# Optimization experiments

Measured on AMD Instinct MI355X. Metric: run time of the kernel, lower is better.

Reference implementation:

```python
import jax, jax.numpy as jnp
import numpy as np

BATCH = 4096
INDIM = 1024
OUTDIM = 1024
NNZ = 52224  # min(1024,1024) * int(1024 * 0.05)


def setup_inputs() -> dict:
    key = jax.random.key(0)
    k1, k2, k3, k4, k5 = jax.random.split(key, 5)
    stdv = np.sqrt(2.0 / INDIM).astype(np.float32)
    input_ = jax.random.normal(k1, (BATCH, INDIM), dtype=jnp.float32)
    weight = jax.random.normal(k2, (NNZ,), dtype=jnp.float32) * stdv
    bias = jax.random.normal(k3, (OUTDIM,), dtype=jnp.float32) * stdv
    ind_in = jax.random.randint(k4, (NNZ,), 0, INDIM, dtype=jnp.int32)
    ind_out = jax.random.randint(k5, (NNZ,), 0, OUTDIM, dtype=jnp.int32)
    return {"input_": input_, "weight": weight, "bias": bias,
            "ind_in": ind_in, "ind_out": ind_out}


def reference(input_, weight, bias, ind_in, ind_out):
    # x = input_[:, ind_in] * weight        [B, NNZ]
    gathered = input_[:, ind_in] * weight
    # scatter_add into output columns       [B, OUTDIM]
    out = jnp.zeros((input_.shape[0], OUTDIM), dtype=input_.dtype)
    out = out.at[:, ind_out].add(gathered)
    return out + bias
```

## Files before the change

### kernel.cpp

```cpp
#include <hip/hip_runtime.h>
#include <stdint.h>

#define INDIM   1024
#define OUTDIM  1024
#define BM 64
#define BN 64
#define BK 64
#define KTILES (INDIM / BK)

typedef __attribute__((ext_vector_type(8))) short  short8;
typedef __attribute__((ext_vector_type(4))) float  floatx4;

__global__ void k_scatter_w(const int* __restrict__ ind_in, const int* __restrict__ ind_out,
                            const float* __restrict__ w, float* __restrict__ W32T, int nnz) {
    int k = blockIdx.x * 256 + threadIdx.x;
    if (k < nnz)
        atomicAdd(&W32T[(size_t)ind_out[k] * INDIM + ind_in[k]], w[k]);
}

__device__ __forceinline__ uint32_t bf16pack(float x, float y) {
    uint32_t ux = __float_as_uint(x);
    ux = ((ux + 0x7FFFu + ((ux >> 16) & 1u)) >> 16) & 0xFFFFu;
    uint32_t uy = __float_as_uint(y);
    uy = (uy + 0x7FFFu + ((uy >> 16) & 1u)) & 0xFFFF0000u;
    return ux | uy;
}

__global__ void k_convert(const float4* __restrict__ A, uint2* __restrict__ A16, int nA4,
                          const float4* __restrict__ Wt, uint2* __restrict__ W16, int nW4) {
    int i = blockIdx.x * 256 + threadIdx.x;
    int stride = gridDim.x * 256;
    for (int j = i; j < nA4; j += stride) {
        float4 v = A[j];
        A16[j] = make_uint2(bf16pack(v.x, v.y), bf16pack(v.z, v.w));
    }
    for (int j = i; j < nW4; j += stride) {
        float4 v = Wt[j];
        W16[j] = make_uint2(bf16pack(v.x, v.y), bf16pack(v.z, v.w));
    }
}

__global__ __launch_bounds__(256, 4) void k_gemm(
    const ushort* __restrict__ A16,
    const ushort* __restrict__ W16T,
    const float* __restrict__ bias,
    float* __restrict__ C, int M)
{
    __shared__ ushort lA[BM * BK];
    __shared__ ushort lB[BN * BK];

    const int t      = threadIdx.x;
    const int w      = t >> 6;
    const int L      = t & 63;
    const int lane15 = L & 15;
    const int lane7  = L & 7;
    const int quad   = L >> 4;
    const int wm     = w >> 1, wn = w & 1;

    const int bid = blockIdx.x;
    const int bm0 = ((bid & 7) * 8 + (bid >> 7)) * BM;
    const int bn0 = ((bid >> 3) & 15) * BN;

    const int srow = t >> 3;
    const int j8   = (t & 7) ^ (srow & 7);

    const ushort* Abase = A16  + (size_t)bm0 * INDIM;
    const ushort* Bbase = W16T + (size_t)bn0 * INDIM;

    floatx4 acc[2][2] = {};

    for (int kt = 0; kt < KTILES; ++kt) {
        const int gcol = kt * BK + j8 * 8;
        uint4 va0 = *(const uint4*)(Abase + (size_t)srow        * INDIM + gcol);
        uint4 va1 = *(const uint4*)(Abase + (size_t)(srow + 32) * INDIM + gcol);
        uint4 vb0 = *(const uint4*)(Bbase + (size_t)srow        * INDIM + gcol);
        uint4 vb1 = *(const uint4*)(Bbase + (size_t)(srow + 32) * INDIM + gcol);
        __syncthreads();
        *(uint4*)(lA + (size_t)t * 8)         = va0;
        *(uint4*)(lA + (size_t)(t + 256) * 8) = va1;
        *(uint4*)(lB + (size_t)t * 8)         = vb0;
        *(uint4*)(lB + (size_t)(t + 256) * 8) = vb1;
        __syncthreads();

        #pragma unroll
        for (int ks = 0; ks < 2; ++ks) {
            const int koff = (((ks * 4 + quad) ^ lane7) * 8);
            short8 af[2], bf[2];
            #pragma unroll
            for (int tm = 0; tm < 2; ++tm)
                af[tm] = *(const short8*)(lA + (wm * 32 + tm * 16 + lane15) * 64 + koff);
            #pragma unroll
            for (int tn = 0; tn < 2; ++tn)
                bf[tn] = *(const short8*)(lB + (wn * 32 + tn * 16 + lane15) * 64 + koff);
            #pragma unroll
            for (int tm = 0; tm < 2; ++tm)
                #pragma unroll
                for (int tn = 0; tn < 2; ++tn)
                    acc[tm][tn] = __builtin_amdgcn_mfma_f32_16x16x32_bf16(
                        af[tm], bf[tn], acc[tm][tn], 0, 0, 0);
        }
    }

    #pragma unroll
    for (int tm = 0; tm < 2; ++tm) {
        #pragma unroll
        for (int tn = 0; tn < 2; ++tn) {
            const int col = bn0 + wn * 32 + tn * 16 + lane15;
            const float bv = bias[col];
            #pragma unroll
            for (int r = 0; r < 4; ++r) {
                const int row = bm0 + wm * 32 + tm * 16 + quad * 4 + r;
                C[(size_t)row * OUTDIM + col] = acc[tm][tn][r] + bv;
            }
        }
    }
}

extern "C" void kernel_launch(void* const* d_in, const int* in_sizes, int n_in,
                              void* d_out, int out_size, void* d_ws, size_t ws_size,
                              hipStream_t stream) {
    const float* input  = (const float*)d_in[0];
    const float* weight = (const float*)d_in[1];
    const float* bias   = (const float*)d_in[2];
    const int*   ind_in  = (const int*)d_in[3];
    const int*   ind_out = (const int*)d_in[4];
    float* out = (float*)d_out;

    const int nnz = in_sizes[1];
    const int M   = out_size / OUTDIM;

    char* ws = (char*)d_ws;
    float*  W32T = (float*)ws;
    ushort* W16T = (ushort*)(ws + (4u << 20));
    ushort* A16  = (ushort*)(ws + (6u << 20));

    (void)hipMemsetAsync(W32T, 0, (size_t)OUTDIM * INDIM * sizeof(float), stream);
    k_scatter_w<<<(nnz + 255) / 256, 256, 0, stream>>>(ind_in, ind_out, weight, W32T, nnz);
    k_convert<<<2048, 256, 0, stream>>>((const float4*)input, (uint2*)A16, M * INDIM / 4,
                                        (const float4*)W32T, (uint2*)W16T, OUTDIM * INDIM / 4);
    k_gemm<<<(M / BM) * (OUTDIM / BN), 256, 0, stream>>>(A16, W16T, bias, out, M);
}
```

Measured before the change: 99.61 us.

## Fuse weight scatter and bf16 conversion via grid barrier; use direct-to-LDS loads

Merges the scatter-add and the conversion kernels into one persistent-style kernel of 1024 blocks. The blocks synchronise through a global atomic counter barrier, which removes one launch. The GEMM now stages tiles with global_load_lds, so data goes straight to LDS without passing through registers, and the output uses nontemporal stores. The grid barrier requires all 1024 blocks to be co-resident, and it assumes nnz fits within the 256K threads.

```diff
diff --git a/kernel.cpp b/kernel.cpp
--- a/kernel.cpp
+++ b/kernel.cpp
@@ -7,16 +7,10 @@
 #define BN 64
 #define BK 64
 #define KTILES (INDIM / BK)
+#define PREP_BLOCKS 1024
 
 typedef __attribute__((ext_vector_type(8))) short  short8;
 typedef __attribute__((ext_vector_type(4))) float  floatx4;
-
-__global__ void k_scatter_w(const int* __restrict__ ind_in, const int* __restrict__ ind_out,
-                            const float* __restrict__ w, float* __restrict__ W32T, int nnz) {
-    int k = blockIdx.x * 256 + threadIdx.x;
-    if (k < nnz)
-        atomicAdd(&W32T[(size_t)ind_out[k] * INDIM + ind_in[k]], w[k]);
-}
 
 __device__ __forceinline__ uint32_t bf16pack(float x, float y) {
     uint32_t ux = __float_as_uint(x);
@@ -26,18 +20,42 @@
     return ux | uy;
 }
 
-__global__ void k_convert(const float4* __restrict__ A, uint2* __restrict__ A16, int nA4,
-                          const float4* __restrict__ Wt, uint2* __restrict__ W16, int nW4) {
-    int i = blockIdx.x * 256 + threadIdx.x;
-    int stride = gridDim.x * 256;
-    for (int j = i; j < nA4; j += stride) {
-        float4 v = A[j];
+__global__ __launch_bounds__(256) void k_prep(
+    const int* __restrict__ ind_in, const int* __restrict__ ind_out,
+    const float* __restrict__ wgt, int nnz,
+    const float4* __restrict__ A32, int nA4,
+    float* __restrict__ W32T, uint2* __restrict__ W16T, uint2* __restrict__ A16,
+    unsigned* __restrict__ barrier_ctr)
+{
+    const int gtid = blockIdx.x * 256 + threadIdx.x;
+
+    if (gtid < nnz)
+        atomicAdd(&W32T[(size_t)ind_out[gtid] * INDIM + ind_in[gtid]], wgt[gtid]);
+
+    __threadfence();
+    __syncthreads();
+    if (threadIdx.x == 0) {
+        __hip_atomic_fetch_add(barrier_ctr, 1u, __ATOMIC_RELEASE, __HIP_MEMORY_SCOPE_AGENT);
+        while (__hip_atomic_load(barrier_ctr, __ATOMIC_ACQUIRE, __HIP_MEMORY_SCOPE_AGENT)
+               < (unsigned)PREP_BLOCKS)
+            __builtin_amdgcn_s_sleep(4);
+    }
+    __syncthreads();
+
+    {
+        float4 v = ((const float4*)W32T)[gtid];
+        W16T[gtid] = make_uint2(bf16pack(v.x, v.y), bf16pack(v.z, v.w));
+    }
+    for (int j = gtid; j < nA4; j += PREP_BLOCKS * 256) {
+        float4 v = A32[j];
         A16[j] = make_uint2(bf16pack(v.x, v.y), bf16pack(v.z, v.w));
     }
-    for (int j = i; j < nW4; j += stride) {
-        float4 v = Wt[j];
-        W16[j] = make_uint2(bf16pack(v.x, v.y), bf16pack(v.z, v.w));
-    }
+}
+
+__device__ __forceinline__ void gload_lds16(const ushort* g, ushort* l) {
+    __builtin_amdgcn_global_load_lds(
+        (const __attribute__((address_space(1))) void*)g,
+        (__attribute__((address_space(3))) void*)l, 16, 0, 0);
 }
 
 __global__ __launch_bounds__(256, 4) void k_gemm(
@@ -67,19 +85,20 @@
     const ushort* Abase = A16  + (size_t)bm0 * INDIM;
     const ushort* Bbase = W16T + (size_t)bn0 * INDIM;
 
+    ushort* dA0 = lA + w * 512;
+    ushort* dA1 = lA + 2048 + w * 512;
+    ushort* dB0 = lB + w * 512;
+    ushort* dB1 = lB + 2048 + w * 512;
+
     floatx4 acc[2][2] = {};
 
     for (int kt = 0; kt < KTILES; ++kt) {
         const int gcol = kt * BK + j8 * 8;
-        uint4 va0 = *(const uint4*)(Abase + (size_t)srow        * INDIM + gcol);
-        uint4 va1 = *(const uint4*)(Abase + (size_t)(srow + 32) * INDIM + gcol);
-        uint4 vb0 = *(const uint4*)(Bbase + (size_t)srow        * INDIM + gcol);
-        uint4 vb1 = *(const uint4*)(Bbase + (size_t)(srow + 32) * INDIM + gcol);
         __syncthreads();
-        *(uint4*)(lA + (size_t)t * 8)         = va0;
-        *(uint4*)(lA + (size_t)(t + 256) * 8) = va1;
-        *(uint4*)(lB + (size_t)t * 8)         = vb0;
-        *(uint4*)(lB + (size_t)(t + 256) * 8) = vb1;
+        gload_lds16(Abase + (size_t)srow        * INDIM + gcol, dA0);
+        gload_lds16(Abase + (size_t)(srow + 32) * INDIM + gcol, dA1);
+        gload_lds16(Bbase + (size_t)srow        * INDIM + gcol, dB0);
+        gload_lds16(Bbase + (size_t)(srow + 32) * INDIM + gcol, dB1);
         __syncthreads();
 
         #pragma unroll
@@ -110,7 +129,8 @@
             #pragma unroll
             for (int r = 0; r < 4; ++r) {
                 const int row = bm0 + wm * 32 + tm * 16 + quad * 4 + r;
-                C[(size_t)row * OUTDIM + col] = acc[tm][tn][r] + bv;
+                __builtin_nontemporal_store(acc[tm][tn][r] + bv,
+                                            &C[(size_t)row * OUTDIM + col]);
             }
         }
     }
@@ -128,15 +148,17 @@
 
     const int nnz = in_sizes[1];
     const int M   = out_size / OUTDIM;
+    const int nA4 = M * INDIM / 4;
 
     char* ws = (char*)d_ws;
-    float*  W32T = (float*)ws;
-    ushort* W16T = (ushort*)(ws + (4u << 20));
-    ushort* A16  = (ushort*)(ws + (6u << 20));
+    float*    W32T = (float*)ws;
+    unsigned* ctr  = (unsigned*)(ws + (4u << 20));
+    ushort*   W16T = (ushort*)(ws + (4u << 20) + 4096);
+    ushort*   A16  = (ushort*)(ws + (6u << 20) + 4096);
 
-    (void)hipMemsetAsync(W32T, 0, (size_t)OUTDIM * INDIM * sizeof(float), stream);
-    k_scatter_w<<<(nnz + 255) / 256, 256, 0, stream>>>(ind_in, ind_out, weight, W32T, nnz);
-    k_convert<<<2048, 256, 0, stream>>>((const float4*)input, (uint2*)A16, M * INDIM / 4,
-                                        (const float4*)W32T, (uint2*)W16T, OUTDIM * INDIM / 4);
+    (void)hipMemsetAsync(ws, 0, (4u << 20) + 4096, stream);
+    k_prep<<<PREP_BLOCKS, 256, 0, stream>>>(ind_in, ind_out, weight, nnz,
+                                            (const float4*)input, nA4,
+                                            W32T, (uint2*)W16T, (uint2*)A16, ctr);
     k_gemm<<<(M / BM) * (OUTDIM / BN), 256, 0, stream>>>(A16, W16T, bias, out, M);
 }
```

New measurement: 228.5 us. +129.4%, slower.
